# Optimization experiments

Measured on AMD Instinct MI355X. Metric: run time of the kernel, lower is better.

## Reference

```python
import jax, jax.numpy as jnp
import numpy as np

B, T, NH, HS = 2, 2048, 16, 64
C = NH * HS
V_SHIFT = 1          # value shift; queries start at position V_SHIFT
EXP_SCALE = 10.0     # exp_param_scale
KB_UP = 5.0          # kernel_beta_upbound


def setup_inputs() -> dict:
    key = jax.random.key(0)
    ks = jax.random.split(key, 8)
    s = 0.02
    return {
        "x": jax.random.normal(ks[0], (B, T, C), jnp.float32),
        # leaky-average key path: linear proj + per-head decay coefficient
        "W_la": jax.random.normal(ks[1], (C, C), jnp.float32) * s,
        "la_coef": jax.random.uniform(ks[2], (NH,), jnp.float32, 0.1, 0.9),
        "kernel_beta": jnp.ones((NH,), jnp.float32) / EXP_SCALE,
        "value_beta": jnp.ones((NH,), jnp.float32) * (-0.5) / EXP_SCALE,
        # value featurizer (lowrlinearconv): linear + per-head mixing coef
        "W_v": jax.random.normal(ks[3], (C, C), jnp.float32) * s,
        "v_coef": jax.random.uniform(ks[4], (NH,), jnp.float32, 0.0, 1.0),
        "W_proj": jax.random.normal(ks[5], (C, C), jnp.float32) * s,
    }


def reference(x, W_la, la_coef, kernel_beta, value_beta, W_v, v_coef, W_proj):
    B_, T_, C_ = x.shape
    # ---- keys: leaky average (per-head EMA recurrence) of linear projection ----
    xl = (x @ W_la).reshape(B_, T_, NH, HS)          # (B,T,nh,hs)
    alpha = la_coef.reshape(NH, 1)                   # per-head decay

    def step(carry, xt):  # carry,xt: (B,nh,hs)
        new = alpha * carry + (1.0 - alpha) * xt
        return new, new

    _, kt = jax.lax.scan(step, jnp.zeros((B_, NH, HS), x.dtype),
                         jnp.swapaxes(xl, 0, 1))    # (T,B,nh,hs)
    k = jnp.transpose(kt, (1, 2, 0, 3))              # (B,nh,T,hs)
    k = k / jnp.linalg.norm(k, axis=-1, keepdims=True)
    kb = jnp.exp(jnp.minimum(kernel_beta * EXP_SCALE, KB_UP)).reshape(1, NH, 1, 1)
    k = k * kb

    # ---- values: lowrlinearconv featurizer (shift=1, kernel=2) + L2 norm ----
    xv = (x @ W_v).reshape(B_, T_, NH, HS).transpose(0, 2, 1, 3)   # (B,nh,T,hs)
    xv_sh = jnp.concatenate([xv[:, :, 1:], jnp.zeros_like(xv[:, :, :1])], axis=2)
    c = v_coef.reshape(1, NH, 1, 1)
    v = xv_sh * (1.0 - c) + xv * c
    v = v / jnp.linalg.norm(v, axis=-1, keepdims=True)
    v = v * jnp.exp(value_beta * EXP_SCALE).reshape(1, NH, 1, 1)

    # ---- shifted-causal masked SDPA (scale=1); queries are positions >= V_SHIFT ----
    q = k[:, :, V_SHIFT:]                            # (B,nh,T-1,hs)
    scores = jnp.einsum('bhqd,bhkd->bhqk', q, k)
    qpos = jnp.arange(V_SHIFT, T_)[:, None]
    kpos = jnp.arange(T_)[None, :]
    mask = kpos < qpos                               # key j visible iff j < query position
    scores = jnp.where(mask, scores, -jnp.inf)
    att = jax.nn.softmax(scores, axis=-1)
    y_att = jnp.einsum('bhqk,bhkd->bhqd', att, v)
    y = jnp.concatenate([jnp.zeros((B_, NH, V_SHIFT, HS), x.dtype), y_att], axis=2)
    y = jnp.transpose(y, (0, 2, 1, 3)).reshape(B_, T_, C_)
    return y @ W_proj                                # dropouts are eval-mode identity
```

## Files before the change

### kernel.cpp

```cpp
#include <hip/hip_runtime.h>
#include <hip/hip_bf16.h>

#define B_  2
#define T_  2048
#define NH_ 16
#define HS_ 64
#define C_  1024
#define SCL_ 128
#define SCN_ (T_ / SCL_)
#define NT_  (T_ / 64)
#define TEL_ 4096

typedef __attribute__((ext_vector_type(8))) short bf16x8;
typedef __attribute__((ext_vector_type(4))) float f32x4;

__device__ inline int pack_bf16(float a, float b) {
  union { __hip_bfloat16 h; unsigned short u; } ua, ub;
  ua.h = __float2bfloat16(a);
  ub.h = __float2bfloat16(b);
  return (int)(((unsigned)ub.u << 16) | (unsigned)ua.u);
}

__device__ inline void gl_lds16(const __hip_bfloat16* g, __hip_bfloat16* l) {
  __builtin_amdgcn_global_load_lds(
      (const __attribute__((address_space(1))) unsigned int*)g,
      (__attribute__((address_space(3))) unsigned int*)l, 16, 0, 0);
}

__global__ __launch_bounds__(256) void prep1_kernel(const float* __restrict__ x,
                                                    const float* __restrict__ W_la,
                                                    const float* __restrict__ W_v,
                                                    const float* __restrict__ W_proj,
                                                    __hip_bfloat16* __restrict__ x16,
                                                    __hip_bfloat16* __restrict__ Wcat,
                                                    __hip_bfloat16* __restrict__ WprojT) {
  __shared__ __hip_bfloat16 tile[64][66];
  const int bid = (int)blockIdx.x;
  if (bid < 2048) {
    const int i = (bid * 256 + (int)threadIdx.x) * 8;
    const float4 a = *reinterpret_cast<const float4*>(x + i);
    const float4 b = *reinterpret_cast<const float4*>(x + i + 4);
    union { int s[4]; int4 v; } u;
    u.s[0] = pack_bf16(a.x, a.y);
    u.s[1] = pack_bf16(a.z, a.w);
    u.s[2] = pack_bf16(b.x, b.y);
    u.s[3] = pack_bf16(b.z, b.w);
    *reinterpret_cast<int4*>(x16 + i) = u.v;
    return;
  }
  const int id = bid - 2048;
  const int z = id >> 8;
  const int rem = id & 255;
  const int bx = rem & 15, by = rem >> 4;
  const float* W = (z == 0) ? W_la : (z == 1) ? W_v : W_proj;
  __hip_bfloat16* WT = (z == 2) ? WprojT : Wcat + (size_t)z * C_ * C_;
  const int w = threadIdx.x >> 6, l = threadIdx.x & 63;
  const int n0 = bx * 64, k0 = by * 64;
#pragma unroll
  for (int r = 0; r < 16; ++r) {
    const int k = k0 + w * 16 + r;
    tile[w * 16 + r][l] = __float2bfloat16(W[(size_t)k * C_ + n0 + l]);
  }
  __syncthreads();
#pragma unroll
  for (int r = 0; r < 16; ++r) {
    const int nn = w * 16 + r;
    WT[(size_t)(n0 + nn) * C_ + k0 + l] = tile[l][nn];
  }
}

__global__ __launch_bounds__(256) void gemm_in_kernel(const __hip_bfloat16* __restrict__ A,
                                                      const __hip_bfloat16* __restrict__ BT,
                                                      float* __restrict__ C0,
                                                      float* __restrict__ C1) {
  __shared__ __hip_bfloat16 As[2 * 128 * 32];
  __shared__ __hip_bfloat16 Bs[2 * 128 * 32];
  const int tid = threadIdx.x;
  const int m0 = blockIdx.y * 128, n0 = blockIdx.x * 128;
  const int w = tid >> 6, l = tid & 63;
  const int n = l & 15, kg = l >> 4;
  const int m0w = (w & 1) * 64, n0w = (w >> 1) * 64;

  const int r0 = tid >> 2, o0 = (tid & 3) * 8;
  const __hip_bfloat16* ag0 = A + (size_t)(m0 + r0) * C_ + o0;
  const __hip_bfloat16* ag1 = A + (size_t)(m0 + 64 + r0) * C_ + o0;
  const __hip_bfloat16* bg0 = BT + (size_t)(n0 + r0) * C_ + o0;
  const __hip_bfloat16* bg1 = BT + (size_t)(n0 + 64 + r0) * C_ + o0;

  f32x4 acc[4][4];
#pragma unroll
  for (int i = 0; i < 4; ++i)
#pragma unroll
    for (int j = 0; j < 4; ++j) acc[i][j] = f32x4{0.f, 0.f, 0.f, 0.f};

  auto stage = [&](int kk, int buf) {
    __hip_bfloat16* a = As + buf * 4096;
    __hip_bfloat16* b = Bs + buf * 4096;
    gl_lds16(ag0 + kk, a + tid * 8);
    gl_lds16(ag1 + kk, a + 2048 + tid * 8);
    gl_lds16(bg0 + kk, b + tid * 8);
    gl_lds16(bg1 + kk, b + 2048 + tid * 8);
  };

  stage(0, 0);
  int cur = 0;
  for (int k0 = 0; k0 < C_; k0 += 32) {
    asm volatile("" ::: "memory");
    __builtin_amdgcn_s_barrier();
    asm volatile("" ::: "memory");
    if (k0 + 32 < C_) {
      stage(k0 + 32, cur ^ 1);
      asm volatile("s_waitcnt vmcnt(4)" ::: "memory");
    } else {
      asm volatile("s_waitcnt vmcnt(0)" ::: "memory");
    }
    __builtin_amdgcn_s_barrier();
    asm volatile("" ::: "memory");

    const __hip_bfloat16* Ab = As + cur * 4096;
    const __hip_bfloat16* Bb = Bs + cur * 4096;
    bf16x8 af[4], bf[4];
#pragma unroll
    for (int ms = 0; ms < 4; ++ms)
      af[ms] = *reinterpret_cast<const bf16x8*>(Ab + (m0w + ms * 16 + n) * 32 + kg * 8);
#pragma unroll
    for (int ns = 0; ns < 4; ++ns)
      bf[ns] = *reinterpret_cast<const bf16x8*>(Bb + (n0w + ns * 16 + n) * 32 + kg * 8);
#pragma unroll
    for (int ms = 0; ms < 4; ++ms)
#pragma unroll
      for (int ns = 0; ns < 4; ++ns)
        acc[ms][ns] = __builtin_amdgcn_mfma_f32_16x16x32_bf16(af[ms], bf[ns], acc[ms][ns], 0, 0, 0);
    cur ^= 1;
  }

  float* Cb = (n0 < C_) ? C0 : C1;
  const int nc = (n0 < C_) ? n0 : n0 - C_;
#pragma unroll
  for (int ms = 0; ms < 4; ++ms) {
#pragma unroll
    for (int r = 0; r < 4; ++r) {
      const int row = m0 + m0w + ms * 16 + kg * 4 + r;
      float* cp = Cb + (size_t)row * C_ + nc + n0w + n;
#pragma unroll
      for (int ns = 0; ns < 4; ++ns) cp[ns * 16] = acc[ms][ns][r];
    }
  }
}

__global__ __launch_bounds__(256) void gemm_proj_kernel(const __hip_bfloat16* __restrict__ A,
                                                        const __hip_bfloat16* __restrict__ BT,
                                                        float* __restrict__ Cout) {
  __shared__ __hip_bfloat16 As[2 * 64 * 32];
  __shared__ __hip_bfloat16 Bs[2 * 128 * 32];
  const int tid = threadIdx.x;
  const int m0 = blockIdx.y * 64, n0 = blockIdx.x * 128;
  const int w = tid >> 6, l = tid & 63;
  const int n = l & 15, kg = l >> 4;

  const int r0 = tid >> 2, o0 = (tid & 3) * 8;
  const __hip_bfloat16* ag = A + (size_t)(m0 + r0) * C_ + o0;
  const __hip_bfloat16* bg0 = BT + (size_t)(n0 + r0) * C_ + o0;
  const __hip_bfloat16* bg1 = BT + (size_t)(n0 + 64 + r0) * C_ + o0;

  f32x4 acc[4][2];
#pragma unroll
  for (int i = 0; i < 4; ++i)
#pragma unroll
    for (int j = 0; j < 2; ++j) acc[i][j] = f32x4{0.f, 0.f, 0.f, 0.f};

  auto stage = [&](int kk, int buf) {
    __hip_bfloat16* a = As + buf * 2048;
    __hip_bfloat16* b = Bs + buf * 4096;
    gl_lds16(ag + kk, a + tid * 8);
    gl_lds16(bg0 + kk, b + tid * 8);
    gl_lds16(bg1 + kk, b + 2048 + tid * 8);
  };

  stage(0, 0);
  int cur = 0;
  for (int k0 = 0; k0 < C_; k0 += 32) {
    asm volatile("" ::: "memory");
    __builtin_amdgcn_s_barrier();
    asm volatile("" ::: "memory");
    if (k0 + 32 < C_) {
      stage(k0 + 32, cur ^ 1);
      asm volatile("s_waitcnt vmcnt(3)" ::: "memory");
    } else {
      asm volatile("s_waitcnt vmcnt(0)" ::: "memory");
    }
    __builtin_amdgcn_s_barrier();
    asm volatile("" ::: "memory");

    const __hip_bfloat16* Ab = As + cur * 2048;
    const __hip_bfloat16* Bb = Bs + cur * 4096;
    bf16x8 af[4], bf[2];
#pragma unroll
    for (int ms = 0; ms < 4; ++ms)
      af[ms] = *reinterpret_cast<const bf16x8*>(Ab + (ms * 16 + n) * 32 + kg * 8);
#pragma unroll
    for (int ns = 0; ns < 2; ++ns)
      bf[ns] = *reinterpret_cast<const bf16x8*>(Bb + (w * 32 + ns * 16 + n) * 32 + kg * 8);
#pragma unroll
    for (int ms = 0; ms < 4; ++ms)
#pragma unroll
      for (int ns = 0; ns < 2; ++ns)
        acc[ms][ns] = __builtin_amdgcn_mfma_f32_16x16x32_bf16(af[ms], bf[ns], acc[ms][ns], 0, 0, 0);
    cur ^= 1;
  }

#pragma unroll
  for (int ms = 0; ms < 4; ++ms) {
#pragma unroll
    for (int r = 0; r < 4; ++r) {
      const int row = m0 + ms * 16 + kg * 4 + r;
      float* cp = Cout + (size_t)row * C_ + n0 + w * 32 + n;
#pragma unroll
      for (int ns = 0; ns < 2; ++ns) cp[ns * 16] = acc[ms][ns][r];
    }
  }
}

__global__ __launch_bounds__(256) void prep2_kernel(const float* __restrict__ xv,
                                                    const float* __restrict__ xl,
                                                    __hip_bfloat16* __restrict__ vt,
                                                    __hip_bfloat16* __restrict__ kb16,
                                                    const float* __restrict__ value_beta,
                                                    const float* __restrict__ v_coef,
                                                    const float* __restrict__ la_coef,
                                                    const float* __restrict__ kernel_beta) {
  __shared__ float4 smem4[2048];
  __shared__ float carrW[4][64];
  __shared__ float carrS[4][64];
  const int bid = (int)blockIdx.x;
  if (bid < 1024) {
    float* cache = reinterpret_cast<float*>(smem4);
    __hip_bfloat16 (*tile)[66] =
        reinterpret_cast<__hip_bfloat16(*)[66]>(reinterpret_cast<char*>(smem4) + 16640);
    const int tc = bid % NT_;
    const int bh = bid / NT_;
    const int h = bh % NH_, b = bh / NH_;
    const int t0 = tc * 64;
    const int tid = threadIdx.x;
    const int w = tid >> 6, l = tid & 63;

    const float c = v_coef[h];
    const float vb = expf(value_beta[h] * 10.0f);

    const float4* xv4 = reinterpret_cast<const float4*>(xv);
    float4* cache4 = reinterpret_cast<float4*>(cache);
#pragma unroll
    for (int i = 0; i < 5; ++i) {
      const int idx = tid + i * 256;
      if (idx < 65 * 16) {
        const int row = idx >> 4, c4 = idx & 15;
        const int t = t0 + row;
        float4 v = {0.f, 0.f, 0.f, 0.f};
        if (t < T_) v = xv4[((size_t)b * T_ + t) * (C_ / 4) + h * (HS_ / 4) + c4];
        cache4[row * 16 + c4] = v;
      }
    }
    __syncthreads();

    for (int r = 0; r < 16; ++r) {
      const int tl = w * 16 + r;
      const float cu = cache[tl * HS_ + l];
      const float nxt = cache[(tl + 1) * HS_ + l];
      float val = nxt * (1.0f - c) + cu * c;
      float ssum = val * val;
#pragma unroll
      for (int m = 32; m; m >>= 1) ssum += __shfl_xor(ssum, m);
      tile[tl][l] = __float2bfloat16(val * (vb / sqrtf(ssum)));
    }
    __syncthreads();
    __hip_bfloat16* vtb = vt + (size_t)(bh * NT_ + tc) * TEL_;
    const int kk = l >> 3, j = l & 7;
    for (int rr = 0; rr < 16; ++rr) {
      const int hs = w * 16 + rr;
      vtb[(kk * 64 + hs) * 8 + j] = tile[l][hs];
    }
    return;
  }
  {
    float* buf = reinterpret_cast<float*>(smem4);
    const int idx = bid - 1024;
    const int c = idx % SCN_;
    const int bh = idx / SCN_;
    const int b = bh / NH_, h = bh % NH_;
    const int tid = threadIdx.x;
    const int w = tid >> 6, l = tid & 63;

    const float alpha = la_coef[h];
    const float onema = 1.0f - alpha;
    const float a32 = __powf(alpha, 32.0f);
    const float kbs = expf(fminf(kernel_beta[h] * 10.0f, 5.0f));
    const float4* src4 = reinterpret_cast<const float4*>(xl + (size_t)b * T_ * C_ + h * HS_);
    float4* buf4 = reinterpret_cast<float4*>(buf);

    auto stageChunk = [&](int t0s) {
#pragma unroll
      for (int i = 0; i < 8; ++i) {
        const int ix = tid + i * 256;
        const int tt = ix >> 4, d4 = ix & 15;
        buf4[tt * 16 + d4] = src4[(size_t)(t0s + tt) * (C_ / 4) + d4];
      }
    };
    auto localCarry = [&]() -> float {
      float A = 0.0f;
      const float* bp = buf + (w * 32) * HS_ + l;
#pragma unroll 8
      for (int tt = 0; tt < 32; ++tt) A = alpha * A + onema * bp[tt * HS_];
      return A;
    };

    float W = 0.0f;
    if (c > 0) {
      stageChunk((c - 1) * SCL_);
      __syncthreads();
      carrW[w][l] = localCarry();
      __syncthreads();
      W = ((carrW[0][l] * a32 + carrW[1][l]) * a32 + carrW[2][l]) * a32 + carrW[3][l];
    }
    const int t0 = c * SCL_;
    __syncthreads();
    stageChunk(t0);
    __syncthreads();
    carrS[w][l] = localCarry();
    __syncthreads();
    float P = W;
#pragma unroll
    for (int j2 = 0; j2 < 3; ++j2)
      if (j2 < w) P = carrS[j2][l] + a32 * P;
    __hip_bfloat16* kt = kb16 + (size_t)bh * NT_ * TEL_;
    const int g = l >> 3, j = l & 7;
    const float* bp = buf + (w * 32) * HS_ + l;
    float A = P;
    for (int rr = 0; rr < 32; ++rr) {
      A = alpha * A + onema * bp[rr * HS_];
      float ss = A * A;
#pragma unroll
      for (int m = 32; m; m >>= 1) ss += __shfl_xor(ss, m);
      const int t = t0 + w * 32 + rr;
      const int tile = t >> 6, key = t & 63;
      kt[(size_t)tile * TEL_ + (g * 64 + key) * 8 + j] = __float2bfloat16(A * (kbs / sqrtf(ss)));
    }
  }
}

__global__ __launch_bounds__(256, 4) void attn_mfma_kernel(
    const __hip_bfloat16* __restrict__ kb,
    const __hip_bfloat16* __restrict__ vt,
    __hip_bfloat16* __restrict__ y) {
  __shared__ __hip_bfloat16 Ks[2][2 * TEL_];
  __shared__ __hip_bfloat16 Ps[4][16 * 64];

  const int id = (int)blockIdx.x;
  const int xcd = id & 7;
  const int s = id >> 3;
  const int bh = xcd + 8 * (s & 3);
  const int v = s >> 2;
  const int qt = (v < 16) ? (31 - v) : (v - 16);
  const int b = bh / NH_, h = bh % NH_;
  const int q0 = qt * 64;
  const int w = threadIdx.x >> 6;
  const int l = threadIdx.x & 63;
  const int n = l & 15;
  const int kg = l >> 4;
  const int qq = w * 16 + n;
  const int query = q0 + qq;
  const int lo = l * 8;
  const int tb = bh * NT_;
  const int so = w * 1024 + lo;

  bf16x8 qf0, qf1;
  {
    const __hip_bfloat16* qtile = kb + (size_t)(tb + qt) * TEL_;
    qf0 = *reinterpret_cast<const bf16x8*>(qtile + (kg * 64 + qq) * 8);
    qf1 = *reinterpret_cast<const bf16x8*>(qtile + ((kg + 4) * 64 + qq) * 8);
  }
  const __hip_bfloat16* vbase = vt + (size_t)tb * TEL_ + (kg * 64 + n) * 8;

  f32x4 accO[4];
#pragma unroll
  for (int i = 0; i < 4; ++i) accO[i] = f32x4{0.f, 0.f, 0.f, 0.f};
  float l_acc = 0.0f;

  __hip_bfloat16* Pw = Ps[w];
  int* Pwi = reinterpret_cast<int*>(Pw);

  auto stage2 = [&](int j0, int buf) {
    const size_t tg = (size_t)(tb + j0) * TEL_;
    __hip_bfloat16* Kb = &Ks[buf][0];
    gl_lds16(kb + tg + so, Kb + so);
    gl_lds16(kb + tg + so + 512, Kb + so + 512);
    gl_lds16(kb + tg + TEL_ + so, Kb + TEL_ + so);
    gl_lds16(kb + tg + TEL_ + so + 512, Kb + TEL_ + so + 512);
  };
  auto stage1 = [&](int j0, int buf) {
    const size_t tg = (size_t)(tb + j0) * TEL_;
    __hip_bfloat16* Kb = &Ks[buf][0];
    gl_lds16(kb + tg + so, Kb + so);
    gl_lds16(kb + tg + so + 512, Kb + so + 512);
  };
  auto loadV = [&](int jt, bf16x8 (&vf)[2][4]) {
    const __hip_bfloat16* vp = vbase + (size_t)jt * TEL_;
#pragma unroll
    for (int ks = 0; ks < 2; ++ks)
#pragma unroll
      for (int mo = 0; mo < 4; ++mo)
        vf[ks][mo] = *reinterpret_cast<const bf16x8*>(vp + ks * 2048 + mo * 128);
  };
  auto computeS = [&](const __hip_bfloat16* Kc, f32x4 (&accS)[4]) {
    __builtin_amdgcn_s_setprio(1);
#pragma unroll
    for (int ms = 0; ms < 4; ++ms) {
      bf16x8 a0 = *reinterpret_cast<const bf16x8*>(Kc + (kg * 64 + ms * 16 + n) * 8);
      bf16x8 a1 = *reinterpret_cast<const bf16x8*>(Kc + ((kg + 4) * 64 + ms * 16 + n) * 8);
      f32x4 z{0.f, 0.f, 0.f, 0.f};
      z = __builtin_amdgcn_mfma_f32_16x16x32_bf16(a0, qf0, z, 0, 0, 0);
      accS[ms] = __builtin_amdgcn_mfma_f32_16x16x32_bf16(a1, qf1, z, 0, 0, 0);
    }
    __builtin_amdgcn_s_setprio(0);
  };
  auto softmaxStore = [&](const f32x4 (&accS)[4], bool diag) {
    if (!diag) {
#pragma unroll
      for (int ms = 0; ms < 4; ++ms) {
        const float p0 = __expf(accS[ms][0]), p1 = __expf(accS[ms][1]);
        const float p2 = __expf(accS[ms][2]), p3 = __expf(accS[ms][3]);
        l_acc += p0 + p1 + p2 + p3;
        const int po = n * 32 + (((ms * 4 + kg) ^ n) << 1);
        int2 pw;
        pw.x = pack_bf16(p0, p1);
        pw.y = pack_bf16(p2, p3);
        *reinterpret_cast<int2*>(&Pwi[po]) = pw;
      }
    } else {
#pragma unroll
      for (int ms = 0; ms < 4; ++ms) {
        const int kbase = ms * 16 + kg * 4;
        float p[4];
#pragma unroll
        for (int r = 0; r < 4; ++r) {
          const float e = __expf(accS[ms][r]);
          p[r] = (kbase + r < qq) ? e : 0.0f;
          l_acc += p[r];
        }
        const int po = n * 32 + (((ms * 4 + kg) ^ n) << 1);
        int2 pw;
        pw.x = pack_bf16(p[0], p[1]);
        pw.y = pack_bf16(p[2], p[3]);
        *reinterpret_cast<int2*>(&Pwi[po]) = pw;
      }
    }
  };
  auto pv = [&](const bf16x8 (&vf)[2][4]) {
    __builtin_amdgcn_s_setprio(1);
#pragma unroll
    for (int ks = 0; ks < 2; ++ks) {
      union { ushort4 u[2]; bf16x8 vv; } pr;
      const int ga = (ks * 8 + kg * 2) ^ n;
      const __hip_bfloat16* pp = Pw + n * 64;
      pr.u[0] = *reinterpret_cast<const ushort4*>(pp + ga * 4);
      pr.u[1] = *reinterpret_cast<const ushort4*>(pp + (ga ^ 1) * 4);
#pragma unroll
      for (int mo = 0; mo < 4; ++mo)
        accO[mo] = __builtin_amdgcn_mfma_f32_16x16x32_bf16(vf[ks][mo], pr.vv, accO[mo], 0, 0, 0);
    }
    __builtin_amdgcn_s_setprio(0);
  };

  if (qt >= 1) stage2(0, 0); else stage1(0, 0);

  int cur = 0;
  int jp = 0;
  for (; jp + 1 <= qt; jp += 2) {
    asm volatile("" ::: "memory");
    __builtin_amdgcn_s_barrier();
    asm volatile("" ::: "memory");

    bf16x8 vfA[2][4];
    loadV(jp, vfA);
    asm volatile("" ::: "memory");

    const int nx = jp + 2;
    if (nx + 1 <= qt) {
      stage2(nx, cur ^ 1);
      asm volatile("s_waitcnt vmcnt(12)" ::: "memory");
    } else if (nx <= qt) {
      stage1(nx, cur ^ 1);
      asm volatile("s_waitcnt vmcnt(10)" ::: "memory");
    } else {
      asm volatile("s_waitcnt vmcnt(8)" ::: "memory");
    }
    __builtin_amdgcn_s_barrier();
    asm volatile("" ::: "memory");

    f32x4 accS[4];
    computeS(&Ks[cur][0], accS);
    softmaxStore(accS, false);
    pv(vfA);

    asm volatile("" ::: "memory");

    bf16x8 vfB[2][4];
    loadV(jp + 1, vfB);
    computeS(&Ks[cur][TEL_], accS);
    softmaxStore(accS, jp + 1 == qt);
    pv(vfB);

    cur ^= 1;
  }
  if (jp <= qt) {
    asm volatile("" ::: "memory");
    __builtin_amdgcn_s_barrier();
    asm volatile("" ::: "memory");
    bf16x8 vfA[2][4];
    loadV(jp, vfA);
    asm volatile("s_waitcnt vmcnt(8)" ::: "memory");
    __builtin_amdgcn_s_barrier();
    asm volatile("" ::: "memory");
    f32x4 accS[4];
    computeS(&Ks[cur][0], accS);
    softmaxStore(accS, true);
    pv(vfA);
  }

  l_acc += __shfl_xor(l_acc, 16);
  l_acc += __shfl_xor(l_acc, 32);
  const float inv = (query == 0) ? 0.0f : 1.0f / l_acc;
  __hip_bfloat16* yb = y + ((size_t)b * T_ + query) * C_ + h * HS_;
#pragma unroll
  for (int mo = 0; mo < 4; ++mo) {
    int2 pkd;
    pkd.x = pack_bf16(accO[mo][0] * inv, accO[mo][1] * inv);
    pkd.y = pack_bf16(accO[mo][2] * inv, accO[mo][3] * inv);
    *reinterpret_cast<int2*>(yb + mo * 16 + kg * 4) = pkd;
  }
}

extern "C" void kernel_launch(void* const* d_in, const int* in_sizes, int n_in,
                              void* d_out, int out_size, void* d_ws, size_t ws_size,
                              hipStream_t stream) {
  const float* x           = (const float*)d_in[0];
  const float* W_la        = (const float*)d_in[1];
  const float* la_coef     = (const float*)d_in[2];
  const float* kernel_beta = (const float*)d_in[3];
  const float* value_beta  = (const float*)d_in[4];
  const float* W_v         = (const float*)d_in[5];
  const float* v_coef      = (const float*)d_in[6];
  const float* W_proj      = (const float*)d_in[7];
  float* out = (float*)d_out;

  char* wsb = (char*)d_ws;
  const size_t MB = 1024u * 1024u;
  __hip_bfloat16* x16    = (__hip_bfloat16*)(wsb);
  __hip_bfloat16* Wcat   = (__hip_bfloat16*)(wsb + 8 * MB);
  __hip_bfloat16* WprojT = (__hip_bfloat16*)(wsb + 12 * MB);
  float* xl              = (float*)(wsb + 16 * MB);
  float* xv              = (float*)(wsb + 32 * MB);
  __hip_bfloat16* kb16   = (__hip_bfloat16*)(wsb + 48 * MB);
  __hip_bfloat16* vt16   = (__hip_bfloat16*)(wsb + 56 * MB);
  __hip_bfloat16* y16    = (__hip_bfloat16*)(wsb + 64 * MB);
  (void)ws_size; (void)in_sizes; (void)n_in; (void)out_size;

  const int M = B_ * T_;

  prep1_kernel<<<dim3(2048 + 768), dim3(256), 0, stream>>>(x, W_la, W_v, W_proj, x16, Wcat, WprojT);
  gemm_in_kernel<<<dim3(2 * C_ / 128, M / 128), dim3(256), 0, stream>>>(x16, Wcat, xl, xv);
  prep2_kernel<<<dim3(1024 + 512), dim3(256), 0, stream>>>(xv, xl, vt16, kb16,
                                                           value_beta, v_coef, la_coef, kernel_beta);
  attn_mfma_kernel<<<dim3(8 * 128), dim3(256), 0, stream>>>(kb16, vt16, y16);
  gemm_proj_kernel<<<dim3(C_ / 128, M / 64), dim3(256), 0, stream>>>(y16, WprojT, out);
}
```

Measured before the change: 189.8 us.

## Shrink prep kernel shared memory by scanning keys in 64-row halves

Cuts the prep kernel's shared memory from a 32KB buffer to about 16.6KB. The key EMA scan now stages 64-row halves with 16-step sub-scans per wave and combines carries using alpha^16 and alpha^64. The value path keeps normalized bf16 values in registers and reuses the same buffer for the transpose tile. The aim is higher occupancy, at the cost of more barriers and extra staging passes over the previous chunk.

```diff
diff --git a/kernel.cpp b/kernel.cpp
--- a/kernel.cpp
+++ b/kernel.cpp
@@ -229,20 +229,18 @@
                                                     const float* __restrict__ v_coef,
                                                     const float* __restrict__ la_coef,
                                                     const float* __restrict__ kernel_beta) {
-  __shared__ float4 smem4[2048];
-  __shared__ float carrW[4][64];
-  __shared__ float carrS[4][64];
+  __shared__ float smemf[65 * 64];
+  __shared__ float carrP[4][64];
   const int bid = (int)blockIdx.x;
+  const int tid = threadIdx.x;
+  const int w = tid >> 6, l = tid & 63;
+
   if (bid < 1024) {
-    float* cache = reinterpret_cast<float*>(smem4);
-    __hip_bfloat16 (*tile)[66] =
-        reinterpret_cast<__hip_bfloat16(*)[66]>(reinterpret_cast<char*>(smem4) + 16640);
+    float* cache = smemf;
     const int tc = bid % NT_;
     const int bh = bid / NT_;
     const int h = bh % NH_, b = bh / NH_;
     const int t0 = tc * 64;
-    const int tid = threadIdx.x;
-    const int w = tid >> 6, l = tid & 63;
 
     const float c = v_coef[h];
     const float vb = expf(value_beta[h] * 10.0f);
@@ -262,6 +260,8 @@
     }
     __syncthreads();
 
+    unsigned short us[16];
+#pragma unroll
     for (int r = 0; r < 16; ++r) {
       const int tl = w * 16 + r;
       const float cu = cache[tl * HS_ + l];
@@ -270,7 +270,18 @@
       float ssum = val * val;
 #pragma unroll
       for (int m = 32; m; m >>= 1) ssum += __shfl_xor(ssum, m);
-      tile[tl][l] = __float2bfloat16(val * (vb / sqrtf(ssum)));
+      union { __hip_bfloat16 hh; unsigned short uu; } cvt;
+      cvt.hh = __float2bfloat16(val * (vb / sqrtf(ssum)));
+      us[r] = cvt.uu;
+    }
+    __syncthreads();
+
+    __hip_bfloat16 (*tile)[66] = reinterpret_cast<__hip_bfloat16(*)[66]>(smemf);
+#pragma unroll
+    for (int r = 0; r < 16; ++r) {
+      union { __hip_bfloat16 hh; unsigned short uu; } cvt;
+      cvt.uu = us[r];
+      tile[w * 16 + r][l] = cvt.hh;
     }
     __syncthreads();
     __hip_bfloat16* vtb = vt + (size_t)(bh * NT_ + tc) * TEL_;
@@ -282,67 +293,83 @@
     return;
   }
   {
-    float* buf = reinterpret_cast<float*>(smem4);
+    float* buf = smemf;
     const int idx = bid - 1024;
     const int c = idx % SCN_;
     const int bh = idx / SCN_;
     const int b = bh / NH_, h = bh % NH_;
-    const int tid = threadIdx.x;
-    const int w = tid >> 6, l = tid & 63;
 
     const float alpha = la_coef[h];
     const float onema = 1.0f - alpha;
-    const float a32 = __powf(alpha, 32.0f);
+    const float a16 = __powf(alpha, 16.0f);
+    const float a32 = a16 * a16;
+    const float a64 = a32 * a32;
     const float kbs = expf(fminf(kernel_beta[h] * 10.0f, 5.0f));
     const float4* src4 = reinterpret_cast<const float4*>(xl + (size_t)b * T_ * C_ + h * HS_);
     float4* buf4 = reinterpret_cast<float4*>(buf);
 
-    auto stageChunk = [&](int t0s) {
-#pragma unroll
-      for (int i = 0; i < 8; ++i) {
+    auto stageHalf = [&](int t0s) {
+#pragma unroll
+      for (int i = 0; i < 4; ++i) {
         const int ix = tid + i * 256;
         const int tt = ix >> 4, d4 = ix & 15;
         buf4[tt * 16 + d4] = src4[(size_t)(t0s + tt) * (C_ / 4) + d4];
       }
     };
-    auto localCarry = [&]() -> float {
+    auto scan16 = [&]() -> float {
       float A = 0.0f;
-      const float* bp = buf + (w * 32) * HS_ + l;
-#pragma unroll 8
-      for (int tt = 0; tt < 32; ++tt) A = alpha * A + onema * bp[tt * HS_];
+      const float* bp = buf + (w * 16) * HS_ + l;
+#pragma unroll 4
+      for (int tt = 0; tt < 16; ++tt) A = alpha * A + onema * bp[tt * HS_];
       return A;
     };
-
+    auto comb = [&]() -> float {
+      return ((carrP[0][l] * a16 + carrP[1][l]) * a16 + carrP[2][l]) * a16 + carrP[3][l];
+    };
+
+    const int t0 = c * SCL_;
     float W = 0.0f;
     if (c > 0) {
-      stageChunk((c - 1) * SCL_);
+      stageHalf(t0 - SCL_);
       __syncthreads();
-      carrW[w][l] = localCarry();
+      carrP[w][l] = scan16();
       __syncthreads();
-      W = ((carrW[0][l] * a32 + carrW[1][l]) * a32 + carrW[2][l]) * a32 + carrW[3][l];
-    }
-    const int t0 = c * SCL_;
-    __syncthreads();
-    stageChunk(t0);
-    __syncthreads();
-    carrS[w][l] = localCarry();
-    __syncthreads();
-    float P = W;
-#pragma unroll
-    for (int j2 = 0; j2 < 3; ++j2)
-      if (j2 < w) P = carrS[j2][l] + a32 * P;
+      const float Cw0 = comb();
+      stageHalf(t0 - SCL_ + 64);
+      __syncthreads();
+      carrP[w][l] = scan16();
+      __syncthreads();
+      W = a64 * Cw0 + comb();
+    }
+
     __hip_bfloat16* kt = kb16 + (size_t)bh * NT_ * TEL_;
     const int g = l >> 3, j = l & 7;
-    const float* bp = buf + (w * 32) * HS_ + l;
-    float A = P;
-    for (int rr = 0; rr < 32; ++rr) {
-      A = alpha * A + onema * bp[rr * HS_];
-      float ss = A * A;
-#pragma unroll
-      for (int m = 32; m; m >>= 1) ss += __shfl_xor(ss, m);
-      const int t = t0 + w * 32 + rr;
-      const int tile = t >> 6, key = t & 63;
-      kt[(size_t)tile * TEL_ + (g * 64 + key) * 8 + j] = __float2bfloat16(A * (kbs / sqrtf(ss)));
+
+    float Shalf = W;
+#pragma unroll
+    for (int hf = 0; hf < 2; ++hf) {
+      __syncthreads();
+      stageHalf(t0 + hf * 64);
+      __syncthreads();
+      carrP[w][l] = scan16();
+      __syncthreads();
+      const float Snext = a64 * Shalf + comb();
+      float P = Shalf;
+#pragma unroll
+      for (int j2 = 0; j2 < 3; ++j2)
+        if (j2 < w) P = carrP[j2][l] + a16 * P;
+      const float* bp = buf + (w * 16) * HS_ + l;
+      float A = P;
+      for (int rr = 0; rr < 16; ++rr) {
+        A = alpha * A + onema * bp[rr * HS_];
+        float ss = A * A;
+#pragma unroll
+        for (int m = 32; m; m >>= 1) ss += __shfl_xor(ss, m);
+        const int t = t0 + hf * 64 + w * 16 + rr;
+        const int tile = t >> 6, key = t & 63;
+        kt[(size_t)tile * TEL_ + (g * 64 + key) * 8 + j] = __float2bfloat16(A * (kbs / sqrtf(ss)));
+      }
+      Shalf = Snext;
     }
   }
 }
```

Result: no change. 186.9 us (-1.6%).
